# Kernel tuning notes

Measured on AMD Instinct MI355X. Metric: run time of the kernel, lower is better.

Reference implementation:

```python
import jax, jax.numpy as jnp
import numpy as np

HID = 256
HEADS = 8
HD = HID // HEADS  # head_dim = 32


def setup_inputs() -> dict:
    key = jax.random.key(0)
    ks = jax.random.split(key, 16)
    B, N = 4, 2048
    s = 0.02
    inp = {
        'x': jax.random.normal(ks[0], (B, N, 4, HID), dtype=jnp.float32),
        'Wq': jax.random.normal(ks[1], (HID, HID), dtype=jnp.float32) * s,
        'bq': jnp.zeros((HID,), jnp.float32),
        'Wk': jax.random.normal(ks[2], (HID, HID), dtype=jnp.float32) * s,
        'bk': jnp.zeros((HID,), jnp.float32),
        'Wv': jax.random.normal(ks[3], (HID, HID), dtype=jnp.float32) * s,
        'bv': jnp.zeros((HID,), jnp.float32),
        'Wvec': jax.random.normal(ks[4], (2 * HID, HID), dtype=jnp.float32) * s,
        'Wo': jax.random.normal(ks[5], (3 * HID, HID), dtype=jnp.float32) * s,
        'bo': jnp.zeros((3 * HID,), jnp.float32),
        'Wg': jax.random.normal(ks[6], (HID, 2 * HID), dtype=jnp.float32) * s,
        'bg': jnp.zeros((HID,), jnp.float32),
        'alpha_dot': jnp.asarray(1.0, jnp.float32),
        'alpha_norm': jnp.asarray(1.0, jnp.float32),
    }
    return inp


def reference(x, Wq, bq, Wk, bk, Wv, bv, Wvec, Wo, bo, Wg, bg, alpha_dot, alpha_norm):
    B, N, _, H = x.shape
    nh, hd = HEADS, HD
    x_scalar = x[:, :, 0]          # (B,N,H)
    vec = x[:, :, 1:]              # (B,N,3,H)

    def lin(a, W, b=None):
        y = a @ W.T
        return y + b if b is not None else y

    # scalar q/k/v -> (B,heads,N,hd)
    q = lin(x_scalar, Wq, bq).reshape(B, N, nh, hd).transpose(0, 2, 1, 3)
    k = lin(x_scalar, Wk, bk).reshape(B, N, nh, hd).transpose(0, 2, 1, 3)
    v = lin(x_scalar, Wv, bv).reshape(B, N, nh, hd).transpose(0, 2, 1, 3)

    # invariant features from vector channels
    vec_proj = lin(vec, Wvec)                  # (B,N,3,2H)
    vec1, vec2 = vec_proj[..., :H], vec_proj[..., H:]
    vec_dot = jnp.sum(vec1 * vec2, axis=-2)    # (B,N,H)
    vec_norm = jnp.linalg.norm(vec, axis=2)    # (B,N,H)

    # equivariant values: (B,heads,N,3*hd)
    vec_v = vec.reshape(B, N, 3, nh, hd).transpose(0, 3, 1, 2, 4).reshape(B, nh, N, 3 * hd)

    # fused attention: one softmax, aggregate scalar v and vector v together
    scale = 1.0 / np.sqrt(hd).astype(np.float32)
    scores = jnp.einsum('bhqd,bhkd->bhqk', q, k) * scale
    attn = jax.nn.softmax(scores, axis=-1)
    v_all = jnp.concatenate([v, vec_v], axis=-1)        # (B,h,N,4*hd)
    out_all = jnp.einsum('bhqk,bhkd->bhqd', attn, v_all)
    out_s, out_v = out_all[..., :hd], out_all[..., hd:]

    x_out = out_s.transpose(0, 2, 1, 3).reshape(B, N, H)
    vec_aggr = out_v.reshape(B, nh, N, 3, hd).transpose(0, 2, 3, 1, 4).reshape(B, N, 3, H)

    invariants = jnp.concatenate([alpha_dot * vec_dot, alpha_norm * vec_norm], axis=-1)
    gate = jax.nn.sigmoid(lin(invariants, Wg, bg))[:, :, None, :]  # (B,N,1,H)
    vec_combined = gate * vec_aggr + vec  # vector_mixing='add', gating=True

    o = lin(x_out, Wo, bo)
    o1, o2, o3 = o[..., :H], o[..., H:2 * H], o[..., 2 * H:]
    x_updated = vec_dot * o1 + vec_norm * o2 + o3

    x_final = jnp.concatenate([x_updated[:, :, None, :], vec_combined], axis=2)  # (B,N,4,H)
    return x_final
```

## Files before the change

kernel.cpp:

```cpp
#include <hip/hip_runtime.h>
#include <cstdint>
#include <cstddef>

#define HIDN 256
#define NHEAD 8
#define HD 32
#define NSEQ 2048
#define QS (0.17677669529663687f * 1.4426950408889634f)

typedef __attribute__((ext_vector_type(8))) short short8;
typedef __attribute__((ext_vector_type(4))) short short4v;
typedef __attribute__((ext_vector_type(4))) float f32x4;
typedef __attribute__((ext_vector_type(16))) float f32x16;
typedef __attribute__((ext_vector_type(4))) uint32_t u32x4;

static __device__ __forceinline__ short f2bf(float f) {
    union { float f; uint32_t u; } v; v.f = f;
    uint32_t r = (v.u + 0x7FFF + ((v.u >> 16) & 1)) >> 16;
    return (short)r;
}
static __device__ __forceinline__ float bf2f(short s) {
    union { uint32_t u; float f; } v; v.u = ((uint32_t)(uint16_t)s) << 16;
    return v.f;
}

static __device__ __forceinline__ float ex2(float x) {
#if defined(__has_builtin)
#if __has_builtin(__builtin_amdgcn_exp2f)
    return __builtin_amdgcn_exp2f(x);
#else
    return exp2f(x);
#endif
#else
    return exp2f(x);
#endif
}

static __device__ __forceinline__ uint32_t pkbf16(float lo, float hi) {
    uint32_t r;
    asm("v_cvt_pk_bf16_f32 %0, %1, %2" : "=v"(r) : "v"(lo), "v"(hi));
    return r;
}

static __device__ __forceinline__ void gload16(const void* g, void* l) {
    __builtin_amdgcn_global_load_lds(
        (__attribute__((address_space(1))) void*)g,
        (__attribute__((address_space(3))) void*)l, 16, 0, 0);
}

static __device__ __forceinline__ f32x16 zero16() {
    f32x16 z;
    #pragma unroll
    for (int i = 0; i < 16; i++) z[i] = 0.f;
    return z;
}

__global__ __launch_bounds__(256) void wcvt_kernel(
    const float* __restrict__ Wq, const float* __restrict__ Wk,
    const float* __restrict__ Wv, const float* __restrict__ Wvec,
    const float* __restrict__ Wo, const float* __restrict__ Wg,
    const float* __restrict__ bq, const float* __restrict__ bk,
    const float* __restrict__ bv,
    const float* __restrict__ ad, const float* __restrict__ an,
    short* __restrict__ Wqkvb, short* __restrict__ Wvecb,
    short* __restrict__ Wob, short* __restrict__ Wgb, float* __restrict__ bqkvs)
{
    int idx = blockIdx.x * 256 + threadIdx.x;
    if (idx < 65536)        Wqkvb[idx] = f2bf(Wq[idx] * QS);
    else if (idx < 131072)  Wqkvb[idx] = f2bf(Wk[idx - 65536]);
    else if (idx < 196608)  Wqkvb[idx] = f2bf(Wv[idx - 131072]);
    else if (idx < 327680)  Wvecb[idx - 196608] = f2bf(Wvec[idx - 196608]);
    else if (idx < 524288)  Wob[idx - 327680] = f2bf(Wo[idx - 327680]);
    else {
        int i2 = idx - 524288;
        int k = i2 & 511;
        float s = (k < 256) ? ad[0] : an[0];
        Wgb[i2] = f2bf(Wg[i2] * s);
    }
    if (idx < 256)          bqkvs[idx] = bq[idx] * QS;
    else if (idx < 512)     bqkvs[idx] = bk[idx - 256];
    else if (idx < 768)     bqkvs[idx] = bv[idx - 512];
}

__global__ __launch_bounds__(256) void qkv_kernel(
    const float* __restrict__ x, const short* __restrict__ Wqkvb,
    const float* __restrict__ bqkvs,
    short* __restrict__ qbf, short* __restrict__ kbf, short* __restrict__ vtb)
{
    __shared__ short xs[32 * 264];
    __shared__ short vtmp[256 * 34];
    const int tid = threadIdx.x;
    const int D = blockIdx.x;
    const int y = D >> 8;
    const int m0 = (D & 255) * 32;
    const int b  = m0 >> 11;
    const int n0 = m0 & 2047;

    #pragma unroll
    for (int l = 0; l < 8; l++) {
        int i = l * 256 + tid;
        int t = i >> 6, j4 = i & 63;
        float4 v = *(const float4*)(x + (size_t)(m0 + t) * 1024 + j4 * 4);
        short4v s = { f2bf(v.x), f2bf(v.y), f2bf(v.z), f2bf(v.w) };
        *(short4v*)&xs[t * 264 + j4 * 4] = s;
    }
    __syncthreads();

    const int wave = tid >> 6, lane = tid & 63;
    const int col = lane & 15, quad = lane >> 4;

    short8 xf[2][8];
    #pragma unroll
    for (int mt = 0; mt < 2; mt++)
        #pragma unroll
        for (int kk = 0; kk < 8; kk++)
            xf[mt][kk] = *(const short8*)&xs[(mt * 16 + col) * 264 + kk * 32 + quad * 8];

    f32x4 acc[2][4];
    #pragma unroll
    for (int mt = 0; mt < 2; mt++)
        #pragma unroll
        for (int nt = 0; nt < 4; nt++) acc[mt][nt] = (f32x4){0.f,0.f,0.f,0.f};

    const short* Wb = Wqkvb + (size_t)(y * 256 + wave * 64) * 256;
    #pragma unroll
    for (int kk = 0; kk < 8; kk++) {
        #pragma unroll
        for (int nt = 0; nt < 4; nt++) {
            short8 wf = *(const short8*)(Wb + (size_t)(nt * 16 + col) * 256 + kk * 32 + quad * 8);
            #pragma unroll
            for (int mt = 0; mt < 2; mt++)
                acc[mt][nt] = __builtin_amdgcn_mfma_f32_16x16x32_bf16(wf, xf[mt][kk], acc[mt][nt], 0, 0, 0);
        }
    }

    if (y == 0) {
        #pragma unroll
        for (int nt = 0; nt < 4; nt++) {
            int ch = wave * 64 + nt * 16 + quad * 4;
            float4 bi = *(const float4*)&bqkvs[ch];
            int h = ch >> 5, d = ch & 31;
            #pragma unroll
            for (int mt = 0; mt < 2; mt++) {
                int n = n0 + mt * 16 + col;
                short4v s = { f2bf(acc[mt][nt][0] + bi.x), f2bf(acc[mt][nt][1] + bi.y),
                              f2bf(acc[mt][nt][2] + bi.z), f2bf(acc[mt][nt][3] + bi.w) };
                *(short4v*)(qbf + ((size_t)(b * 8 + h) * 2048 + n) * 32 + d) = s;
            }
        }
    } else if (y == 1) {
        #pragma unroll
        for (int nt = 0; nt < 4; nt++) {
            int ch = wave * 64 + nt * 16 + quad * 4;
            float4 bi = *(const float4*)&bqkvs[256 + ch];
            int h = ch >> 5, d = ch & 31;
            #pragma unroll
            for (int mt = 0; mt < 2; mt++) {
                int n = n0 + mt * 16 + col;
                short4v s = { f2bf(acc[mt][nt][0] + bi.x), f2bf(acc[mt][nt][1] + bi.y),
                              f2bf(acc[mt][nt][2] + bi.z), f2bf(acc[mt][nt][3] + bi.w) };
                int f  = ((n & 63) >> 5) * 2 + (d >> 4);
                int lk = (n & 31) + (((d >> 3) & 1) << 5);
                short* dst = kbf + ((size_t)(b * 8 + h) * 32 + (n >> 6)) * 2048
                           + f * 512 + lk * 8 + (d & 7);
                *(short4v*)dst = s;
            }
        }
    } else {
        #pragma unroll
        for (int nt = 0; nt < 4; nt++) {
            int ch = wave * 64 + nt * 16 + quad * 4;
            float4 bi = *(const float4*)&bqkvs[512 + ch];
            #pragma unroll
            for (int mt = 0; mt < 2; mt++) {
                int tok = mt * 16 + col;
                vtmp[(ch + 0) * 34 + tok] = f2bf(acc[mt][nt][0] + bi.x);
                vtmp[(ch + 1) * 34 + tok] = f2bf(acc[mt][nt][1] + bi.y);
                vtmp[(ch + 2) * 34 + tok] = f2bf(acc[mt][nt][2] + bi.z);
                vtmp[(ch + 3) * 34 + tok] = f2bf(acc[mt][nt][3] + bi.w);
            }
        }
        __syncthreads();
        {
            int ch = tid;
            short s[32];
            #pragma unroll
            for (int t = 0; t < 32; t++) s[t] = vtmp[ch * 34 + t];
            int h = ch >> 5, d = ch & 31;
            size_t tile = (size_t)(b * 8 + h) * 32 + (n0 >> 6);
            short* dst = vtb + tile * 8192;
            #pragma unroll
            for (int g = 0; g < 4; g++) {
                int kbse = (n0 & 63) + g * 8;
                int f = kbse >> 4;
                int h2 = (kbse >> 3) & 1;
                *(short8*)(dst + f * 512 + (d + h2 * 32) * 8) = *(short8*)&s[g * 8];
            }
        }
    }
}

__global__ __launch_bounds__(512) void vec_kernel(
    const float* __restrict__ x, const short* __restrict__ Wvecb,
    float* __restrict__ dotb, short* __restrict__ invb,
    float* __restrict__ normb, short* __restrict__ vtb)
{
    __shared__ short vb[3 * 16 * 264];
    const int tid = threadIdx.x;
    const int m0 = blockIdx.x * 16;
    const int b = m0 >> 11, n0 = m0 & 2047;

    #pragma unroll
    for (int p = 0; p < 6; p++) {
        int f4 = p * 512 + tid;
        int t = f4 / 192;
        int rem = f4 - t * 192;
        int c = rem >> 6, j4 = rem & 63;
        float4 v = *(const float4*)(x + (size_t)(m0 + t) * 1024 + 256 + c * 256 + j4 * 4);
        short4v s = { f2bf(v.x), f2bf(v.y), f2bf(v.z), f2bf(v.w) };
        *(short4v*)&vb[(c * 16 + t) * 264 + j4 * 4] = s;
    }
    __syncthreads();

    const int wave = tid >> 6, lane = tid & 63;
    const int col = lane & 15, quad = lane >> 4;
    const int j0 = wave * 32;

    f32x4 d1[3][2], d2[3][2];
    #pragma unroll
    for (int c = 0; c < 3; c++)
        #pragma unroll
        for (int nt = 0; nt < 2; nt++) {
            d1[c][nt] = (f32x4){0.f,0.f,0.f,0.f};
            d2[c][nt] = (f32x4){0.f,0.f,0.f,0.f};
        }

    #pragma unroll
    for (int kk = 0; kk < 8; kk++) {
        short8 w1[2], w2[2];
        #pragma unroll
        for (int nt = 0; nt < 2; nt++) {
            w1[nt] = *(const short8*)&Wvecb[(size_t)(j0 + nt * 16 + col) * 256 + kk * 32 + quad * 8];
            w2[nt] = *(const short8*)&Wvecb[(size_t)(256 + j0 + nt * 16 + col) * 256 + kk * 32 + quad * 8];
        }
        #pragma unroll
        for (int c = 0; c < 3; c++) {
            short8 xf = *(const short8*)&vb[(c * 16 + col) * 264 + kk * 32 + quad * 8];
            #pragma unroll
            for (int nt = 0; nt < 2; nt++) {
                d1[c][nt] = __builtin_amdgcn_mfma_f32_16x16x32_bf16(w1[nt], xf, d1[c][nt], 0, 0, 0);
                d2[c][nt] = __builtin_amdgcn_mfma_f32_16x16x32_bf16(w2[nt], xf, d2[c][nt], 0, 0, 0);
            }
        }
    }
    #pragma unroll
    for (int nt = 0; nt < 2; nt++) {
        f32x4 dac = d1[0][nt] * d2[0][nt] + d1[1][nt] * d2[1][nt] + d1[2][nt] * d2[2][nt];
        float4 o = { dac[0], dac[1], dac[2], dac[3] };
        *(float4*)&dotb[(size_t)(m0 + col) * 256 + j0 + nt * 16 + quad * 4] = o;
        short4v s = { f2bf(dac[0]), f2bf(dac[1]), f2bf(dac[2]), f2bf(dac[3]) };
        *(short4v*)&invb[(size_t)(m0 + col) * 512 + j0 + nt * 16 + quad * 4] = s;
    }

    const int j = tid & 255, tp = tid >> 8;
    const int h = j >> 5, d = j & 31;
    #pragma unroll
    for (int t8 = 0; t8 < 8; t8++) {
        int t = tp * 8 + t8;
        float v0 = bf2f(vb[(0 * 16 + t) * 264 + j]);
        float v1 = bf2f(vb[(1 * 16 + t) * 264 + j]);
        float v2 = bf2f(vb[(2 * 16 + t) * 264 + j]);
        float nm = sqrtf(v0 * v0 + v1 * v1 + v2 * v2);
        normb[(size_t)(m0 + t) * 256 + j] = nm;
        invb[(size_t)(m0 + t) * 512 + 256 + j] = f2bf(nm);
    }
    {
        size_t tile = (size_t)(b * 8 + h) * 32 + (n0 >> 6);
        int kbse = (n0 & 63) + tp * 8;
        int ks = kbse >> 4, h2 = (kbse >> 3) & 1;
        #pragma unroll
        for (int c = 0; c < 3; c++) {
            short8 s;
            #pragma unroll
            for (int t8 = 0; t8 < 8; t8++) s[t8] = vb[(c * 16 + tp * 8 + t8) * 264 + j];
            int f = (1 + c) * 4 + ks;
            *(short8*)(vtb + tile * 8192 + f * 512 + (d + h2 * 32) * 8) = s;
        }
    }
}

__global__ __launch_bounds__(512) void attn_kernel(
    const short* __restrict__ qb, const short* __restrict__ kb,
    const short* __restrict__ vtb,
    short* __restrict__ xob, short* __restrict__ ovb)
{
    __shared__ __align__(16) union {
        short Vs[2][2][8192];
        struct { float om[4][8][64][4]; float lm[256]; } m;
    } u;
    const int tid = threadIdx.x;
    const int wave = tid >> 6, lane = tid & 63;
    const int g = wave >> 2;
    const int lwave = wave & 3, lt = tid & 255;
    const int q32 = lane & 31, hi = lane >> 5;

    const int D = blockIdx.x;
    const int slot = D >> 3;
    const int bh = (D & 7) + ((slot & 3) << 3);
    const int qt = slot >> 2;
    const int m0 = qt * 128 + lwave * 32;
    const int b = bh >> 3, h = bh & 7;

    const short* qbase = qb + (size_t)bh * NSEQ * HD;
    const short* ksrc  = kb + (size_t)bh * 32 * 2048;
    const short* vsrc  = vtb + (size_t)bh * 32 * 8192;

    short8 qfrag[2];
    #pragma unroll
    for (int ks = 0; ks < 2; ks++)
        qfrag[ks] = *(const short8*)(qbase + (size_t)(m0 + q32) * 32 + ks * 16 + hi * 8);

    f32x16 o[4];
    #pragma unroll
    for (int dt = 0; dt < 4; dt++) o[dt] = zero16();
    float lrun = 0.f;

    auto STAGEV = [&](int buf, int t) {
        const short* vp = vsrc + (size_t)t * 8192 + lt * 8;
        #pragma unroll
        for (int p = 0; p < 4; p++)
            gload16(vp + p * 2048, &u.Vs[g][buf][p * 2048 + (lt >> 6) * 512]);
    };

    STAGEV(0, g * 16);
    __syncthreads();

    for (int t = 0; t < 16; t++) {
        const int cur = t & 1;
        const int kt = g * 16 + t;

        short8 kf[4];
        #pragma unroll
        for (int f = 0; f < 4; f++)
            kf[f] = *(const short8*)(ksrc + (size_t)kt * 2048 + f * 512 + lane * 8);

        if (t < 15) STAGEV(cur ^ 1, kt + 1);

        #pragma unroll
        for (int tt = 0; tt < 2; tt++) {
            f32x16 a = zero16();
            a = __builtin_amdgcn_mfma_f32_32x32x16_bf16(kf[2*tt+0], qfrag[0], a, 0, 0, 0);
            a = __builtin_amdgcn_mfma_f32_32x32x16_bf16(kf[2*tt+1], qfrag[1], a, 0, 0, 0);

            #pragma unroll
            for (int sx = 0; sx < 2; sx++) {
                float e0 = ex2(a[8*sx+0]), e1 = ex2(a[8*sx+1]);
                float e2 = ex2(a[8*sx+2]), e3 = ex2(a[8*sx+3]);
                float e4 = ex2(a[8*sx+4]), e5 = ex2(a[8*sx+5]);
                float e6 = ex2(a[8*sx+6]), e7 = ex2(a[8*sx+7]);
                lrun += ((e0 + e1) + (e2 + e3)) + ((e4 + e5) + (e6 + e7));
                uint32_t x0 = pkbf16(e0, e1), y0 = pkbf16(e4, e5);
                uint32_t x1 = pkbf16(e2, e3), y1 = pkbf16(e6, e7);
                asm("v_permlane32_swap_b32 %0, %1" : "+v"(x0), "+v"(y0));
                asm("v_permlane32_swap_b32 %0, %1" : "+v"(x1), "+v"(y1));
                u32x4 pv = { x0, x1, y0, y1 };
                short8 pf = __builtin_bit_cast(short8, pv);
                const int s = tt * 2 + sx;
                #pragma unroll
                for (int dt = 0; dt < 4; dt++) {
                    short8 vf = *(const short8*)&u.Vs[g][cur][(dt * 4 + s) * 512 + lane * 8];
                    o[dt] = __builtin_amdgcn_mfma_f32_32x32x16_bf16(vf, pf, o[dt], 0, 0, 0);
                }
            }
        }
        __syncthreads();
    }

    float lpart = lrun + __shfl_xor(lrun, 32);
    float linv = 0.f;
    size_t mg = (size_t)b * 2048 + m0 + q32;

    if (g == 1) {
        #pragma unroll
        for (int dt = 0; dt < 2; dt++)
            #pragma unroll
            for (int q4 = 0; q4 < 4; q4++) {
                f32x4 c = { o[dt][q4*4+0], o[dt][q4*4+1], o[dt][q4*4+2], o[dt][q4*4+3] };
                *(f32x4*)&u.m.om[lwave][dt * 4 + q4][lane][0] = c;
            }
        u.m.lm[lwave * 64 + lane] = lpart;
    }
    __syncthreads();
    if (g == 0) {
        #pragma unroll
        for (int dt = 0; dt < 2; dt++)
            #pragma unroll
            for (int q4 = 0; q4 < 4; q4++) {
                f32x4 c = *(const f32x4*)&u.m.om[lwave][dt * 4 + q4][lane][0];
                o[dt][q4*4+0] += c[0]; o[dt][q4*4+1] += c[1];
                o[dt][q4*4+2] += c[2]; o[dt][q4*4+3] += c[3];
            }
        float l = lpart + u.m.lm[lwave * 64 + lane];
        linv = 1.0f / l;

        short* xr = xob + mg * 256 + h * 32;
        #pragma unroll
        for (int gg = 0; gg < 4; gg++) {
            short4v sv = { f2bf(o[0][4*gg+0] * linv), f2bf(o[0][4*gg+1] * linv),
                           f2bf(o[0][4*gg+2] * linv), f2bf(o[0][4*gg+3] * linv) };
            *(short4v*)(xr + gg * 8 + hi * 4) = sv;
        }
        short* vr = ovb + mg * 768 + h * 32;
        #pragma unroll
        for (int gg = 0; gg < 4; gg++) {
            short4v sv = { f2bf(o[1][4*gg+0] * linv), f2bf(o[1][4*gg+1] * linv),
                           f2bf(o[1][4*gg+2] * linv), f2bf(o[1][4*gg+3] * linv) };
            *(short4v*)(vr + gg * 8 + hi * 4) = sv;
        }
    }
    __syncthreads();
    if (g == 1) {
        #pragma unroll
        for (int dt = 2; dt < 4; dt++)
            #pragma unroll
            for (int q4 = 0; q4 < 4; q4++) {
                f32x4 c = { o[dt][q4*4+0], o[dt][q4*4+1], o[dt][q4*4+2], o[dt][q4*4+3] };
                *(f32x4*)&u.m.om[lwave][(dt - 2) * 4 + q4][lane][0] = c;
            }
    }
    __syncthreads();
    if (g == 0) {
        short* vr = ovb + mg * 768 + h * 32;
        #pragma unroll
        for (int dt = 2; dt < 4; dt++) {
            #pragma unroll
            for (int q4 = 0; q4 < 4; q4++) {
                f32x4 c = *(const f32x4*)&u.m.om[lwave][(dt - 2) * 4 + q4][lane][0];
                o[dt][q4*4+0] += c[0]; o[dt][q4*4+1] += c[1];
                o[dt][q4*4+2] += c[2]; o[dt][q4*4+3] += c[3];
            }
            #pragma unroll
            for (int gg = 0; gg < 4; gg++) {
                short4v sv = { f2bf(o[dt][4*gg+0] * linv), f2bf(o[dt][4*gg+1] * linv),
                               f2bf(o[dt][4*gg+2] * linv), f2bf(o[dt][4*gg+3] * linv) };
                *(short4v*)(vr + (dt - 1) * 256 + gg * 8 + hi * 4) = sv;
            }
        }
    }
}

__global__ __launch_bounds__(512, 4) void ogemm_kernel(
    const float* __restrict__ x, const short* __restrict__ xob,
    const short* __restrict__ invb,
    const float* __restrict__ dotb, const float* __restrict__ normb,
    const short* __restrict__ ovb,
    const short* __restrict__ Wob, const short* __restrict__ Wgb,
    const float* __restrict__ bo, const float* __restrict__ bg,
    float* __restrict__ out)
{
    __shared__ __align__(16) union {
        struct { short inv[16 * 520]; short xo[16 * 264]; } in;
        struct { short gate[16 * 264]; short o[16 * 776]; } ob;
    } u;
    const int tid = threadIdx.x;
    const int M0 = blockIdx.x * 16;

    #pragma unroll
    for (int l = 0; l < 2; l++) {
        int i = l * 512 + tid;
        int m = i >> 6, seg = i & 63;
        *(short8*)&u.in.inv[m * 520 + seg * 8] =
            *(const short8*)(invb + (size_t)(M0 + m) * 512 + seg * 8);
    }
    {
        int m = tid >> 5, seg = tid & 31;
        *(short8*)&u.in.xo[m * 264 + seg * 8] =
            *(const short8*)(xob + (size_t)(M0 + m) * 256 + seg * 8);
    }
    __syncthreads();

    const int wave = tid >> 6, lane = tid & 63;
    const int col = lane & 15, quad = lane >> 4;
    const int cg = wave * 32;
    const int co = wave * 96;

    f32x4 accg[2], acco[6];
    #pragma unroll
    for (int i = 0; i < 2; i++) accg[i] = (f32x4){0.f,0.f,0.f,0.f};
    #pragma unroll
    for (int i = 0; i < 6; i++) acco[i] = (f32x4){0.f,0.f,0.f,0.f};

    #pragma unroll
    for (int kk = 0; kk < 8; kk++) {
        short8 wg0 = *(const short8*)(Wgb + (size_t)(cg + col) * 512 + (2*kk) * 32 + quad * 8);
        short8 wg1 = *(const short8*)(Wgb + (size_t)(cg + 16 + col) * 512 + (2*kk) * 32 + quad * 8);
        short8 wg2 = *(const short8*)(Wgb + (size_t)(cg + col) * 512 + (2*kk+1) * 32 + quad * 8);
        short8 wg3 = *(const short8*)(Wgb + (size_t)(cg + 16 + col) * 512 + (2*kk+1) * 32 + quad * 8);
        short8 wo0 = *(const short8*)(Wob + (size_t)(co + 0*16 + col) * 256 + kk * 32 + quad * 8);
        short8 wo1 = *(const short8*)(Wob + (size_t)(co + 1*16 + col) * 256 + kk * 32 + quad * 8);
        short8 wo2 = *(const short8*)(Wob + (size_t)(co + 2*16 + col) * 256 + kk * 32 + quad * 8);
        short8 wo3 = *(const short8*)(Wob + (size_t)(co + 3*16 + col) * 256 + kk * 32 + quad * 8);
        short8 wo4 = *(const short8*)(Wob + (size_t)(co + 4*16 + col) * 256 + kk * 32 + quad * 8);
        short8 wo5 = *(const short8*)(Wob + (size_t)(co + 5*16 + col) * 256 + kk * 32 + quad * 8);
        short8 xg0 = *(const short8*)&u.in.inv[col * 520 + (2*kk) * 32 + quad * 8];
        short8 xg1 = *(const short8*)&u.in.inv[col * 520 + (2*kk+1) * 32 + quad * 8];
        short8 xoo = *(const short8*)&u.in.xo[col * 264 + kk * 32 + quad * 8];
        __builtin_amdgcn_sched_barrier(0);
        accg[0] = __builtin_amdgcn_mfma_f32_16x16x32_bf16(wg0, xg0, accg[0], 0, 0, 0);
        accg[1] = __builtin_amdgcn_mfma_f32_16x16x32_bf16(wg1, xg0, accg[1], 0, 0, 0);
        accg[0] = __builtin_amdgcn_mfma_f32_16x16x32_bf16(wg2, xg1, accg[0], 0, 0, 0);
        accg[1] = __builtin_amdgcn_mfma_f32_16x16x32_bf16(wg3, xg1, accg[1], 0, 0, 0);
        acco[0] = __builtin_amdgcn_mfma_f32_16x16x32_bf16(wo0, xoo, acco[0], 0, 0, 0);
        acco[1] = __builtin_amdgcn_mfma_f32_16x16x32_bf16(wo1, xoo, acco[1], 0, 0, 0);
        acco[2] = __builtin_amdgcn_mfma_f32_16x16x32_bf16(wo2, xoo, acco[2], 0, 0, 0);
        acco[3] = __builtin_amdgcn_mfma_f32_16x16x32_bf16(wo3, xoo, acco[3], 0, 0, 0);
        acco[4] = __builtin_amdgcn_mfma_f32_16x16x32_bf16(wo4, xoo, acco[4], 0, 0, 0);
        acco[5] = __builtin_amdgcn_mfma_f32_16x16x32_bf16(wo5, xoo, acco[5], 0, 0, 0);
    }
    __syncthreads();

    #pragma unroll
    for (int i = 0; i < 2; i++) {
        int ch = cg + i * 16 + quad * 4;
        float4 bi = *(const float4*)&bg[ch];
        short4v s = { f2bf(1.f / (1.f + __expf(-(accg[i][0] + bi.x)))),
                      f2bf(1.f / (1.f + __expf(-(accg[i][1] + bi.y)))),
                      f2bf(1.f / (1.f + __expf(-(accg[i][2] + bi.z)))),
                      f2bf(1.f / (1.f + __expf(-(accg[i][3] + bi.w)))) };
        *(short4v*)&u.ob.gate[col * 264 + ch] = s;
    }
    #pragma unroll
    for (int i = 0; i < 6; i++) {
        int ch = co + i * 16 + quad * 4;
        float4 bi = *(const float4*)&bo[ch];
        short4v s = { f2bf(acco[i][0] + bi.x), f2bf(acco[i][1] + bi.y),
                      f2bf(acco[i][2] + bi.z), f2bf(acco[i][3] + bi.w) };
        *(short4v*)&u.ob.o[col * 776 + ch] = s;
    }
    __syncthreads();

    #pragma unroll
    for (int l = 0; l < 8; l++) {
        int idx4 = l * 512 + tid;
        int m = idx4 >> 8;
        int j = (idx4 & 255) * 4;
        size_t mg = (size_t)(M0 + m);
        if (j < 256) {
            float4 dv = *(const float4*)(dotb + mg * 256 + j);
            float4 nv = *(const float4*)(normb + mg * 256 + j);
            short4v o1 = *(short4v*)&u.ob.o[m * 776 + j];
            short4v o2 = *(short4v*)&u.ob.o[m * 776 + 256 + j];
            short4v o3 = *(short4v*)&u.ob.o[m * 776 + 512 + j];
            float4 r;
            r.x = dv.x * bf2f(o1[0]) + nv.x * bf2f(o2[0]) + bf2f(o3[0]);
            r.y = dv.y * bf2f(o1[1]) + nv.y * bf2f(o2[1]) + bf2f(o3[1]);
            r.z = dv.z * bf2f(o1[2]) + nv.z * bf2f(o2[2]) + bf2f(o3[2]);
            r.w = dv.w * bf2f(o1[3]) + nv.w * bf2f(o2[3]) + bf2f(o3[3]);
            *(float4*)(out + mg * 1024 + j) = r;
        } else {
            int c = (j >> 8) - 1, jj = j & 255;
            short4v g4 = *(short4v*)&u.ob.gate[m * 264 + jj];
            short4v av4 = *(const short4v*)(ovb + mg * 768 + c * 256 + jj);
            float4 xv = *(const float4*)(x + mg * 1024 + 256 + c * 256 + jj);
            float4 r = { bf2f(g4[0]) * bf2f(av4[0]) + xv.x, bf2f(g4[1]) * bf2f(av4[1]) + xv.y,
                         bf2f(g4[2]) * bf2f(av4[2]) + xv.z, bf2f(g4[3]) * bf2f(av4[3]) + xv.w };
            *(float4*)(out + mg * 1024 + j) = r;
        }
    }
}

extern "C" void kernel_launch(void* const* d_in, const int* in_sizes, int n_in,
                              void* d_out, int out_size, void* d_ws, size_t ws_size,
                              hipStream_t stream)
{
    const float* x    = (const float*)d_in[0];
    const float* Wq   = (const float*)d_in[1];
    const float* bq   = (const float*)d_in[2];
    const float* Wk   = (const float*)d_in[3];
    const float* bk   = (const float*)d_in[4];
    const float* Wv   = (const float*)d_in[5];
    const float* bv   = (const float*)d_in[6];
    const float* Wvec = (const float*)d_in[7];
    const float* Wo   = (const float*)d_in[8];
    const float* bo   = (const float*)d_in[9];
    const float* Wg   = (const float*)d_in[10];
    const float* bg   = (const float*)d_in[11];
    const float* adp  = (const float*)d_in[12];
    const float* anp  = (const float*)d_in[13];
    float* out = (float*)d_out;

    float* ws    = (float*)d_ws;
    short* qbf   = (short*)ws;
    short* kbf   = (short*)(ws + 1048576);
    short* vtb   = (short*)(ws + 2097152);
    float* dotb  = ws + 6291456;
    float* normb = ws + 8388608;
    short* xob   = (short*)(ws + 10485760);
    short* ovb   = (short*)(ws + 11534336);
    short* invb  = (short*)(ws + 17825792);
    short* Wqkvb = (short*)(ws + 19922944);
    float* bqkvs = ws + 20021248;
    short* Wvecb = (short*)(ws + 20022016);
    short* Wob   = (short*)(ws + 20087552);
    short* Wgb   = (short*)(ws + 20185856);

    wcvt_kernel<<<2560, 256, 0, stream>>>(Wq, Wk, Wv, Wvec, Wo, Wg, bq, bk, bv,
                                          adp, anp, Wqkvb, Wvecb, Wob, Wgb, bqkvs);
    qkv_kernel<<<768, 256, 0, stream>>>(x, Wqkvb, bqkvs, qbf, kbf, vtb);
    vec_kernel<<<512, 512, 0, stream>>>(x, Wvecb, dotb, invb, normb, vtb);
    attn_kernel<<<512, 512, 0, stream>>>(qbf, kbf, vtb, xob, ovb);
    ogemm_kernel<<<512, 512, 0, stream>>>(x, xob, invb, dotb, normb, ovb,
                                          Wob, Wgb, bo, bg, out);
}
```

Measured before the change: 234.9 us.

## Merge qkv and vec kernels into one launch; prefetch K fragments in attention

The separate qkv and vec projection kernels become one prep kernel with 1792 blocks of 256 threads. The vec path is split into two half-column blocks and both paths share a single shared-memory buffer. This removes a launch and the gap between the two kernels, and lets independent work overlap on the GPU. The attention inner loop is also unrolled by two with ping-pong K fragment registers, so the next tile's K load is issued alongside the V staging before the current compute. The cost is more register pressure in attention, and the vec path now loads its x tile twice, once per half.

```diff
diff --git a/kernel.cpp b/kernel.cpp
--- a/kernel.cpp
+++ b/kernel.cpp
@@ -82,209 +82,207 @@
     else if (idx < 768)     bqkvs[idx] = bv[idx - 512];
 }
 
-__global__ __launch_bounds__(256) void qkv_kernel(
+__global__ __launch_bounds__(256) void prep_kernel(
     const float* __restrict__ x, const short* __restrict__ Wqkvb,
-    const float* __restrict__ bqkvs,
-    short* __restrict__ qbf, short* __restrict__ kbf, short* __restrict__ vtb)
+    const float* __restrict__ bqkvs, const short* __restrict__ Wvecb,
+    short* __restrict__ qbf, short* __restrict__ kbf, short* __restrict__ vtb,
+    float* __restrict__ dotb, short* __restrict__ invb, float* __restrict__ normb)
 {
-    __shared__ short xs[32 * 264];
-    __shared__ short vtmp[256 * 34];
+    __shared__ __align__(16) short smem[3 * 16 * 264];
     const int tid = threadIdx.x;
     const int D = blockIdx.x;
-    const int y = D >> 8;
-    const int m0 = (D & 255) * 32;
-    const int b  = m0 >> 11;
-    const int n0 = m0 & 2047;
-
-    #pragma unroll
-    for (int l = 0; l < 8; l++) {
-        int i = l * 256 + tid;
-        int t = i >> 6, j4 = i & 63;
-        float4 v = *(const float4*)(x + (size_t)(m0 + t) * 1024 + j4 * 4);
-        short4v s = { f2bf(v.x), f2bf(v.y), f2bf(v.z), f2bf(v.w) };
-        *(short4v*)&xs[t * 264 + j4 * 4] = s;
-    }
-    __syncthreads();
 
     const int wave = tid >> 6, lane = tid & 63;
     const int col = lane & 15, quad = lane >> 4;
 
-    short8 xf[2][8];
-    #pragma unroll
-    for (int mt = 0; mt < 2; mt++)
-        #pragma unroll
-        for (int kk = 0; kk < 8; kk++)
-            xf[mt][kk] = *(const short8*)&xs[(mt * 16 + col) * 264 + kk * 32 + quad * 8];
-
-    f32x4 acc[2][4];
-    #pragma unroll
-    for (int mt = 0; mt < 2; mt++)
-        #pragma unroll
-        for (int nt = 0; nt < 4; nt++) acc[mt][nt] = (f32x4){0.f,0.f,0.f,0.f};
-
-    const short* Wb = Wqkvb + (size_t)(y * 256 + wave * 64) * 256;
-    #pragma unroll
-    for (int kk = 0; kk < 8; kk++) {
-        #pragma unroll
-        for (int nt = 0; nt < 4; nt++) {
-            short8 wf = *(const short8*)(Wb + (size_t)(nt * 16 + col) * 256 + kk * 32 + quad * 8);
-            #pragma unroll
-            for (int mt = 0; mt < 2; mt++)
-                acc[mt][nt] = __builtin_amdgcn_mfma_f32_16x16x32_bf16(wf, xf[mt][kk], acc[mt][nt], 0, 0, 0);
-        }
-    }
-
-    if (y == 0) {
-        #pragma unroll
-        for (int nt = 0; nt < 4; nt++) {
-            int ch = wave * 64 + nt * 16 + quad * 4;
-            float4 bi = *(const float4*)&bqkvs[ch];
-            int h = ch >> 5, d = ch & 31;
-            #pragma unroll
-            for (int mt = 0; mt < 2; mt++) {
-                int n = n0 + mt * 16 + col;
-                short4v s = { f2bf(acc[mt][nt][0] + bi.x), f2bf(acc[mt][nt][1] + bi.y),
-                              f2bf(acc[mt][nt][2] + bi.z), f2bf(acc[mt][nt][3] + bi.w) };
-                *(short4v*)(qbf + ((size_t)(b * 8 + h) * 2048 + n) * 32 + d) = s;
-            }
-        }
-    } else if (y == 1) {
-        #pragma unroll
-        for (int nt = 0; nt < 4; nt++) {
-            int ch = wave * 64 + nt * 16 + quad * 4;
-            float4 bi = *(const float4*)&bqkvs[256 + ch];
-            int h = ch >> 5, d = ch & 31;
-            #pragma unroll
-            for (int mt = 0; mt < 2; mt++) {
-                int n = n0 + mt * 16 + col;
-                short4v s = { f2bf(acc[mt][nt][0] + bi.x), f2bf(acc[mt][nt][1] + bi.y),
-                              f2bf(acc[mt][nt][2] + bi.z), f2bf(acc[mt][nt][3] + bi.w) };
-                int f  = ((n & 63) >> 5) * 2 + (d >> 4);
-                int lk = (n & 31) + (((d >> 3) & 1) << 5);
-                short* dst = kbf + ((size_t)(b * 8 + h) * 32 + (n >> 6)) * 2048
-                           + f * 512 + lk * 8 + (d & 7);
-                *(short4v*)dst = s;
+    if (D < 1024) {
+        const int half = D & 1;
+        const int m0 = (D >> 1) * 16;
+        const int b = m0 >> 11, n0 = m0 & 2047;
+
+        #pragma unroll
+        for (int p = 0; p < 12; p++) {
+            int f4 = p * 256 + tid;
+            int t = f4 / 192;
+            int rem = f4 - t * 192;
+            int c = rem >> 6, j4 = rem & 63;
+            float4 v = *(const float4*)(x + (size_t)(m0 + t) * 1024 + 256 + c * 256 + j4 * 4);
+            short4v s = { f2bf(v.x), f2bf(v.y), f2bf(v.z), f2bf(v.w) };
+            *(short4v*)&smem[(c * 16 + t) * 264 + j4 * 4] = s;
+        }
+        __syncthreads();
+
+        const int j0 = half * 128 + wave * 32;
+
+        f32x4 d1[3][2], d2[3][2];
+        #pragma unroll
+        for (int c = 0; c < 3; c++)
+            #pragma unroll
+            for (int nt = 0; nt < 2; nt++) {
+                d1[c][nt] = (f32x4){0.f,0.f,0.f,0.f};
+                d2[c][nt] = (f32x4){0.f,0.f,0.f,0.f};
+            }
+
+        #pragma unroll
+        for (int kk = 0; kk < 8; kk++) {
+            short8 w1[2], w2[2];
+            #pragma unroll
+            for (int nt = 0; nt < 2; nt++) {
+                w1[nt] = *(const short8*)&Wvecb[(size_t)(j0 + nt * 16 + col) * 256 + kk * 32 + quad * 8];
+                w2[nt] = *(const short8*)&Wvecb[(size_t)(256 + j0 + nt * 16 + col) * 256 + kk * 32 + quad * 8];
+            }
+            #pragma unroll
+            for (int c = 0; c < 3; c++) {
+                short8 xf = *(const short8*)&smem[(c * 16 + col) * 264 + kk * 32 + quad * 8];
+                #pragma unroll
+                for (int nt = 0; nt < 2; nt++) {
+                    d1[c][nt] = __builtin_amdgcn_mfma_f32_16x16x32_bf16(w1[nt], xf, d1[c][nt], 0, 0, 0);
+                    d2[c][nt] = __builtin_amdgcn_mfma_f32_16x16x32_bf16(w2[nt], xf, d2[c][nt], 0, 0, 0);
+                }
+            }
+        }
+        #pragma unroll
+        for (int nt = 0; nt < 2; nt++) {
+            f32x4 dac = d1[0][nt] * d2[0][nt] + d1[1][nt] * d2[1][nt] + d1[2][nt] * d2[2][nt];
+            float4 o = { dac[0], dac[1], dac[2], dac[3] };
+            *(float4*)&dotb[(size_t)(m0 + col) * 256 + j0 + nt * 16 + quad * 4] = o;
+            short4v s = { f2bf(dac[0]), f2bf(dac[1]), f2bf(dac[2]), f2bf(dac[3]) };
+            *(short4v*)&invb[(size_t)(m0 + col) * 512 + j0 + nt * 16 + quad * 4] = s;
+        }
+
+        const int j = half * 128 + (tid & 127);
+        const int tp = tid >> 7;
+        #pragma unroll
+        for (int t8 = 0; t8 < 8; t8++) {
+            int t = tp * 8 + t8;
+            float v0 = bf2f(smem[(0 * 16 + t) * 264 + j]);
+            float v1 = bf2f(smem[(1 * 16 + t) * 264 + j]);
+            float v2 = bf2f(smem[(2 * 16 + t) * 264 + j]);
+            float nm = sqrtf(v0 * v0 + v1 * v1 + v2 * v2);
+            normb[(size_t)(m0 + t) * 256 + j] = nm;
+            invb[(size_t)(m0 + t) * 512 + 256 + j] = f2bf(nm);
+        }
+        {
+            size_t tile = (size_t)(b * 8 + (j >> 5)) * 32 + (n0 >> 6);
+            int kbse = (n0 & 63) + tp * 8;
+            int ks = kbse >> 4, h2 = (kbse >> 3) & 1;
+            #pragma unroll
+            for (int c = 0; c < 3; c++) {
+                short8 s;
+                #pragma unroll
+                for (int t8 = 0; t8 < 8; t8++) s[t8] = smem[(c * 16 + tp * 8 + t8) * 264 + j];
+                int f = (1 + c) * 4 + ks;
+                *(short8*)(vtb + tile * 8192 + f * 512 + ((j & 31) + h2 * 32) * 8) = s;
             }
         }
     } else {
-        #pragma unroll
-        for (int nt = 0; nt < 4; nt++) {
-            int ch = wave * 64 + nt * 16 + quad * 4;
-            float4 bi = *(const float4*)&bqkvs[512 + ch];
-            #pragma unroll
-            for (int mt = 0; mt < 2; mt++) {
-                int tok = mt * 16 + col;
-                vtmp[(ch + 0) * 34 + tok] = f2bf(acc[mt][nt][0] + bi.x);
-                vtmp[(ch + 1) * 34 + tok] = f2bf(acc[mt][nt][1] + bi.y);
-                vtmp[(ch + 2) * 34 + tok] = f2bf(acc[mt][nt][2] + bi.z);
-                vtmp[(ch + 3) * 34 + tok] = f2bf(acc[mt][nt][3] + bi.w);
-            }
+        short* xs   = smem;
+        short* vtmp = smem;
+        const int E = D - 1024;
+        const int y = E >> 8;
+        const int m0 = (E & 255) * 32;
+        const int b  = m0 >> 11;
+        const int n0 = m0 & 2047;
+
+        #pragma unroll
+        for (int l = 0; l < 8; l++) {
+            int i = l * 256 + tid;
+            int t = i >> 6, j4 = i & 63;
+            float4 v = *(const float4*)(x + (size_t)(m0 + t) * 1024 + j4 * 4);
+            short4v s = { f2bf(v.x), f2bf(v.y), f2bf(v.z), f2bf(v.w) };
+            *(short4v*)&xs[t * 264 + j4 * 4] = s;
         }
         __syncthreads();
-        {
-            int ch = tid;
-            short s[32];
-            #pragma unroll
-            for (int t = 0; t < 32; t++) s[t] = vtmp[ch * 34 + t];
-            int h = ch >> 5, d = ch & 31;
-            size_t tile = (size_t)(b * 8 + h) * 32 + (n0 >> 6);
-            short* dst = vtb + tile * 8192;
-            #pragma unroll
-            for (int g = 0; g < 4; g++) {
-                int kbse = (n0 & 63) + g * 8;
-                int f = kbse >> 4;
-                int h2 = (kbse >> 3) & 1;
-                *(short8*)(dst + f * 512 + (d + h2 * 32) * 8) = *(short8*)&s[g * 8];
-            }
-        }
-    }
-}
-
-__global__ __launch_bounds__(512) void vec_kernel(
-    const float* __restrict__ x, const short* __restrict__ Wvecb,
-    float* __restrict__ dotb, short* __restrict__ invb,
-    float* __restrict__ normb, short* __restrict__ vtb)
-{
-    __shared__ short vb[3 * 16 * 264];
-    const int tid = threadIdx.x;
-    const int m0 = blockIdx.x * 16;
-    const int b = m0 >> 11, n0 = m0 & 2047;
-
-    #pragma unroll
-    for (int p = 0; p < 6; p++) {
-        int f4 = p * 512 + tid;
-        int t = f4 / 192;
-        int rem = f4 - t * 192;
-        int c = rem >> 6, j4 = rem & 63;
-        float4 v = *(const float4*)(x + (size_t)(m0 + t) * 1024 + 256 + c * 256 + j4 * 4);
-        short4v s = { f2bf(v.x), f2bf(v.y), f2bf(v.z), f2bf(v.w) };
-        *(short4v*)&vb[(c * 16 + t) * 264 + j4 * 4] = s;
-    }
-    __syncthreads();
-
-    const int wave = tid >> 6, lane = tid & 63;
-    const int col = lane & 15, quad = lane >> 4;
-    const int j0 = wave * 32;
-
-    f32x4 d1[3][2], d2[3][2];
-    #pragma unroll
-    for (int c = 0; c < 3; c++)
-        #pragma unroll
-        for (int nt = 0; nt < 2; nt++) {
-            d1[c][nt] = (f32x4){0.f,0.f,0.f,0.f};
-            d2[c][nt] = (f32x4){0.f,0.f,0.f,0.f};
-        }
-
-    #pragma unroll
-    for (int kk = 0; kk < 8; kk++) {
-        short8 w1[2], w2[2];
-        #pragma unroll
-        for (int nt = 0; nt < 2; nt++) {
-            w1[nt] = *(const short8*)&Wvecb[(size_t)(j0 + nt * 16 + col) * 256 + kk * 32 + quad * 8];
-            w2[nt] = *(const short8*)&Wvecb[(size_t)(256 + j0 + nt * 16 + col) * 256 + kk * 32 + quad * 8];
-        }
-        #pragma unroll
-        for (int c = 0; c < 3; c++) {
-            short8 xf = *(const short8*)&vb[(c * 16 + col) * 264 + kk * 32 + quad * 8];
-            #pragma unroll
-            for (int nt = 0; nt < 2; nt++) {
-                d1[c][nt] = __builtin_amdgcn_mfma_f32_16x16x32_bf16(w1[nt], xf, d1[c][nt], 0, 0, 0);
-                d2[c][nt] = __builtin_amdgcn_mfma_f32_16x16x32_bf16(w2[nt], xf, d2[c][nt], 0, 0, 0);
-            }
-        }
-    }
-    #pragma unroll
-    for (int nt = 0; nt < 2; nt++) {
-        f32x4 dac = d1[0][nt] * d2[0][nt] + d1[1][nt] * d2[1][nt] + d1[2][nt] * d2[2][nt];
-        float4 o = { dac[0], dac[1], dac[2], dac[3] };
-        *(float4*)&dotb[(size_t)(m0 + col) * 256 + j0 + nt * 16 + quad * 4] = o;
-        short4v s = { f2bf(dac[0]), f2bf(dac[1]), f2bf(dac[2]), f2bf(dac[3]) };
-        *(short4v*)&invb[(size_t)(m0 + col) * 512 + j0 + nt * 16 + quad * 4] = s;
-    }
-
-    const int j = tid & 255, tp = tid >> 8;
-    const int h = j >> 5, d = j & 31;
-    #pragma unroll
-    for (int t8 = 0; t8 < 8; t8++) {
-        int t = tp * 8 + t8;
-        float v0 = bf2f(vb[(0 * 16 + t) * 264 + j]);
-        float v1 = bf2f(vb[(1 * 16 + t) * 264 + j]);
-        float v2 = bf2f(vb[(2 * 16 + t) * 264 + j]);
-        float nm = sqrtf(v0 * v0 + v1 * v1 + v2 * v2);
-        normb[(size_t)(m0 + t) * 256 + j] = nm;
-        invb[(size_t)(m0 + t) * 512 + 256 + j] = f2bf(nm);
-    }
-    {
-        size_t tile = (size_t)(b * 8 + h) * 32 + (n0 >> 6);
-        int kbse = (n0 & 63) + tp * 8;
-        int ks = kbse >> 4, h2 = (kbse >> 3) & 1;
-        #pragma unroll
-        for (int c = 0; c < 3; c++) {
-            short8 s;
-            #pragma unroll
-            for (int t8 = 0; t8 < 8; t8++) s[t8] = vb[(c * 16 + tp * 8 + t8) * 264 + j];
-            int f = (1 + c) * 4 + ks;
-            *(short8*)(vtb + tile * 8192 + f * 512 + (d + h2 * 32) * 8) = s;
+
+        short8 xf[2][8];
+        #pragma unroll
+        for (int mt = 0; mt < 2; mt++)
+            #pragma unroll
+            for (int kk = 0; kk < 8; kk++)
+                xf[mt][kk] = *(const short8*)&xs[(mt * 16 + col) * 264 + kk * 32 + quad * 8];
+
+        f32x4 acc[2][4];
+        #pragma unroll
+        for (int mt = 0; mt < 2; mt++)
+            #pragma unroll
+            for (int nt = 0; nt < 4; nt++) acc[mt][nt] = (f32x4){0.f,0.f,0.f,0.f};
+
+        const short* Wb = Wqkvb + (size_t)(y * 256 + wave * 64) * 256;
+        #pragma unroll
+        for (int kk = 0; kk < 8; kk++) {
+            #pragma unroll
+            for (int nt = 0; nt < 4; nt++) {
+                short8 wf = *(const short8*)(Wb + (size_t)(nt * 16 + col) * 256 + kk * 32 + quad * 8);
+                #pragma unroll
+                for (int mt = 0; mt < 2; mt++)
+                    acc[mt][nt] = __builtin_amdgcn_mfma_f32_16x16x32_bf16(wf, xf[mt][kk], acc[mt][nt], 0, 0, 0);
+            }
+        }
+
+        if (y == 0) {
+            #pragma unroll
+            for (int nt = 0; nt < 4; nt++) {
+                int ch = wave * 64 + nt * 16 + quad * 4;
+                float4 bi = *(const float4*)&bqkvs[ch];
+                int h = ch >> 5, d = ch & 31;
+                #pragma unroll
+                for (int mt = 0; mt < 2; mt++) {
+                    int n = n0 + mt * 16 + col;
+                    short4v s = { f2bf(acc[mt][nt][0] + bi.x), f2bf(acc[mt][nt][1] + bi.y),
+                                  f2bf(acc[mt][nt][2] + bi.z), f2bf(acc[mt][nt][3] + bi.w) };
+                    *(short4v*)(qbf + ((size_t)(b * 8 + h) * 2048 + n) * 32 + d) = s;
+                }
+            }
+        } else if (y == 1) {
+            #pragma unroll
+            for (int nt = 0; nt < 4; nt++) {
+                int ch = wave * 64 + nt * 16 + quad * 4;
+                float4 bi = *(const float4*)&bqkvs[256 + ch];
+                int h = ch >> 5, d = ch & 31;
+                #pragma unroll
+                for (int mt = 0; mt < 2; mt++) {
+                    int n = n0 + mt * 16 + col;
+                    short4v s = { f2bf(acc[mt][nt][0] + bi.x), f2bf(acc[mt][nt][1] + bi.y),
+                                  f2bf(acc[mt][nt][2] + bi.z), f2bf(acc[mt][nt][3] + bi.w) };
+                    int f  = ((n & 63) >> 5) * 2 + (d >> 4);
+                    int lk = (n & 31) + (((d >> 3) & 1) << 5);
+                    short* dst = kbf + ((size_t)(b * 8 + h) * 32 + (n >> 6)) * 2048
+                               + f * 512 + lk * 8 + (d & 7);
+                    *(short4v*)dst = s;
+                }
+            }
+        } else {
+            __syncthreads();
+            #pragma unroll
+            for (int nt = 0; nt < 4; nt++) {
+                int ch = wave * 64 + nt * 16 + quad * 4;
+                float4 bi = *(const float4*)&bqkvs[512 + ch];
+                #pragma unroll
+                for (int mt = 0; mt < 2; mt++) {
+                    int tok = mt * 16 + col;
+                    vtmp[(ch + 0) * 34 + tok] = f2bf(acc[mt][nt][0] + bi.x);
+                    vtmp[(ch + 1) * 34 + tok] = f2bf(acc[mt][nt][1] + bi.y);
+                    vtmp[(ch + 2) * 34 + tok] = f2bf(acc[mt][nt][2] + bi.z);
+                    vtmp[(ch + 3) * 34 + tok] = f2bf(acc[mt][nt][3] + bi.w);
+                }
+            }
+            __syncthreads();
+            {
+                int ch = tid;
+                short s[32];
+                #pragma unroll
+                for (int t = 0; t < 32; t++) s[t] = vtmp[ch * 34 + t];
+                int h = ch >> 5, d = ch & 31;
+                size_t tile = (size_t)(b * 8 + h) * 32 + (n0 >> 6);
+                short* dst = vtb + tile * 8192;
+                #pragma unroll
+                for (int g = 0; g < 4; g++) {
+                    int kbse = (n0 & 63) + g * 8;
+                    int f = kbse >> 4;
+                    int h2 = (kbse >> 3) & 1;
+                    *(short8*)(dst + f * 512 + (d + h2 * 32) * 8) = *(short8*)&s[g * 8];
+                }
+            }
         }
     }
 }
@@ -332,25 +330,20 @@
             gload16(vp + p * 2048, &u.Vs[g][buf][p * 2048 + (lt >> 6) * 512]);
     };
 
-    STAGEV(0, g * 16);
-    __syncthreads();
-
-    for (int t = 0; t < 16; t++) {
-        const int cur = t & 1;
-        const int kt = g * 16 + t;
-
-        short8 kf[4];
-        #pragma unroll
-        for (int f = 0; f < 4; f++)
-            kf[f] = *(const short8*)(ksrc + (size_t)kt * 2048 + f * 512 + lane * 8);
-
-        if (t < 15) STAGEV(cur ^ 1, kt + 1);
-
+    short8 kfA[4], kfB[4];
+
+    auto BODY = [&](int kt, int buf, short8 (&kfU)[4], short8 (&kfP)[4], bool pre) {
+        if (pre) {
+            STAGEV(buf ^ 1, kt + 1);
+            #pragma unroll
+            for (int f = 0; f < 4; f++)
+                kfP[f] = *(const short8*)(ksrc + (size_t)(kt + 1) * 2048 + f * 512 + lane * 8);
+        }
         #pragma unroll
         for (int tt = 0; tt < 2; tt++) {
             f32x16 a = zero16();
-            a = __builtin_amdgcn_mfma_f32_32x32x16_bf16(kf[2*tt+0], qfrag[0], a, 0, 0, 0);
-            a = __builtin_amdgcn_mfma_f32_32x32x16_bf16(kf[2*tt+1], qfrag[1], a, 0, 0, 0);
+            a = __builtin_amdgcn_mfma_f32_32x32x16_bf16(kfU[2*tt+0], qfrag[0], a, 0, 0, 0);
+            a = __builtin_amdgcn_mfma_f32_32x32x16_bf16(kfU[2*tt+1], qfrag[1], a, 0, 0, 0);
 
             #pragma unroll
             for (int sx = 0; sx < 2; sx++) {
@@ -368,12 +361,24 @@
                 const int s = tt * 2 + sx;
                 #pragma unroll
                 for (int dt = 0; dt < 4; dt++) {
-                    short8 vf = *(const short8*)&u.Vs[g][cur][(dt * 4 + s) * 512 + lane * 8];
+                    short8 vf = *(const short8*)&u.Vs[g][buf][(dt * 4 + s) * 512 + lane * 8];
                     o[dt] = __builtin_amdgcn_mfma_f32_32x32x16_bf16(vf, pf, o[dt], 0, 0, 0);
                 }
             }
         }
         __syncthreads();
+    };
+
+    #pragma unroll
+    for (int f = 0; f < 4; f++)
+        kfA[f] = *(const short8*)(ksrc + (size_t)(g * 16) * 2048 + f * 512 + lane * 8);
+    STAGEV(0, g * 16);
+    __syncthreads();
+
+    for (int t2 = 0; t2 < 8; t2++) {
+        const int kt0 = g * 16 + t2 * 2;
+        BODY(kt0,     0, kfA, kfB, true);
+        BODY(kt0 + 1, 1, kfB, kfA, t2 < 7);
     }
 
     float lpart = lrun + __shfl_xor(lrun, 32);
@@ -606,8 +611,8 @@
 
     wcvt_kernel<<<2560, 256, 0, stream>>>(Wq, Wk, Wv, Wvec, Wo, Wg, bq, bk, bv,
                                           adp, anp, Wqkvb, Wvecb, Wob, Wgb, bqkvs);
-    qkv_kernel<<<768, 256, 0, stream>>>(x, Wqkvb, bqkvs, qbf, kbf, vtb);
-    vec_kernel<<<512, 512, 0, stream>>>(x, Wvecb, dotb, invb, normb, vtb);
+    prep_kernel<<<1792, 256, 0, stream>>>(x, Wqkvb, bqkvs, Wvecb,
+                                          qbf, kbf, vtb, dotb, invb, normb);
     attn_kernel<<<512, 512, 0, stream>>>(qbf, kbf, vtb, xob, ovb);
     ogemm_kernel<<<512, 512, 0, stream>>>(x, xob, invb, dotb, normb, ovb,
                                           Wob, Wgb, bo, bg, out);
```

New measurement: 247.2 us. 5.3% more time.
